# Performance work log

Hardware: AMD Instinct MI355X
Metric: run time of the kernel (lower is better)

The kernel has to match this reference:

```python
import jax, jax.numpy as jnp
import numpy as np

EPS = 1e-10
TOP_K = 2  # experts_per_token


def setup_inputs() -> dict:
    key = jax.random.key(0)
    k1, k2 = jax.random.split(key)
    dim, E = 2048, 64
    B, S = 4, 4096
    x = jax.random.normal(k1, (B * S, dim), dtype=jnp.float32)
    W = jax.random.normal(k2, (dim, E), dtype=jnp.float32) * (1.0 / np.sqrt(dim))
    b = jnp.zeros((E,), dtype=jnp.float32)
    return {"x": x, "W": W, "b": b, "batch_size": B, "seq_len": S}


def reference(x, W, b, batch_size, seq_len):
    E = W.shape[1]
    N = x.shape[0]  # batch_size * seq_len
    # gate + softmax + clamp
    scores = jax.nn.softmax(x @ W + b, axis=1)
    scores = jnp.clip(scores, EPS, 1.0 - EPS)
    # log-odds transform and rz loss over (seq, experts) per batch
    logits = jnp.log(scores / (1.0 - scores)).reshape(batch_size, seq_len, E)
    rz_loss = jnp.mean(jax.scipy.special.logsumexp(logits, axis=(1, 2)))
    # top-k experts per token
    top_scores, sel_idx = jax.lax.top_k(scores, TOP_K)  # (N, K) each
    flat_idx = sel_idx.reshape(-1)  # (N*K,)
    # histogram of assignments per expert (torch.histc with unit bins)
    num_tokens_per_expert = jax.ops.segment_sum(
        jnp.ones_like(flat_idx, dtype=jnp.float32), flat_idx, num_segments=E)
    # stable argsort groups slots by expert id, preserving token order
    perm = jnp.argsort(flat_idx, stable=True)  # (N*K,)
    top_scores_sorted = top_scores.reshape(-1)[perm]
    token_indices_experts_sorted = perm // TOP_K
    return (top_scores_sorted, token_indices_experts_sorted,
            num_tokens_per_expert, rz_loss)
```

## Files before the change

kernel.cpp:

```cpp
#include <hip/hip_runtime.h>
#include <math.h>

#define EPS_ 1e-10f
#define MARGIN 4e-3f

typedef __attribute__((ext_vector_type(8))) short sh8;
typedef __attribute__((ext_vector_type(4))) float fx4;

__device__ __forceinline__ bool betterf(float v, int i, float w, int j) {
    return (v > w) || (v == w && i < j);
}
__device__ __forceinline__ bool betterd(double v, int i, double w, int j) {
    return (v > w) || (v == w && i < j);
}
__device__ __forceinline__ unsigned short f2bf(float f) {
    unsigned u = __float_as_uint(f);
    u += 0x7fffu + ((u >> 16) & 1u);
    return (unsigned short)(u >> 16);
}
__device__ __forceinline__ float bf2f(unsigned short h) {
    return __uint_as_float(((unsigned)h) << 16);
}
__device__ __forceinline__ void cvt8(const float4 a, const float4 c, sh8& hi, sh8& lo) {
    const float v[8] = {a.x, a.y, a.z, a.w, c.x, c.y, c.z, c.w};
#pragma unroll
    for (int j = 0; j < 8; ++j) {
        const unsigned short h = f2bf(v[j]);
        hi[j] = (short)h;
        lo[j] = (short)f2bf(v[j] - bf2f(h));
    }
}
__device__ __forceinline__ void gload_lds16(const void* g, void* l) {
    __builtin_amdgcn_global_load_lds(
        (const __attribute__((address_space(1))) void*)g,
        (__attribute__((address_space(3))) void*)l, 16, 0, 0);
}

__global__ __launch_bounds__(256)
void wconv(const float* __restrict__ W, unsigned short* __restrict__ wf)
{
    const int gid = blockIdx.x * 256 + threadIdx.x;
    const int e = gid & 63, k = gid >> 6;
    const int s = k >> 5, kk = k & 31, bq = kk >> 3, j = kk & 7;
    const int t = e >> 4, n = e & 15;
    const int l = n + 16 * bq;
    const float w = W[(size_t)k * 64 + e];
    const unsigned short hi = f2bf(w);
    const unsigned short lo = f2bf(w - bf2f(hi));
    const size_t base = ((size_t)s * 4 + t) * 2;
    wf[(base + 0) * 512 + l * 8 + j] = hi;
    wf[(base + 1) * 512 + l * 8 + j] = lo;
}

#define KSPL 4
__global__ __launch_bounds__(256, 4)
void gemm_mfma(const float* __restrict__ x, const unsigned short* __restrict__ wfg,
               int dim, int N, float* __restrict__ zpart)
{
    __shared__ __align__(16) char xs[2][8192];
    __shared__ __align__(16) char wls[2][8192];

    const int tid  = threadIdx.x;
    const int lane = tid & 63;
    const int wv   = tid >> 6;
    const int rgs  = N / 64;
    const int ks   = blockIdx.x / rgs;
    const int rg   = blockIdx.x % rgs;
    const int r0   = rg * 64;
    const int kslice = dim / KSPL;
    const int k0   = ks * kslice;
    const int nstep = kslice / 32;

    const int m = lane & 15;
    const int q = lane >> 4;
    const int arow = wv * 16 + m;
    const int mk = m & 7;

    const int srow_in = lane >> 3;
    const int sgc     = (lane & 7) ^ (srow_in & 7);

    fx4 acc[4] = {};

    const char* wbytes = (const char*)wfg;
    const size_t wstep0 = (size_t)(k0 >> 5) * 8192;

#pragma unroll
    for (int r = 0; r < 2; ++r) {
        const int row = wv * 16 + r * 8 + srow_in;
        gload_lds16(x + (size_t)(r0 + row) * dim + k0 + sgc * 4,
                    &xs[0][(wv * 16 + r * 8) * 128]);
        gload_lds16(wbytes + wstep0 + wv * 2048 + r * 1024 + lane * 16,
                    &wls[0][wv * 2048 + r * 1024]);
    }
    __syncthreads();

    for (int s = 0; s < nstep; ++s) {
        const int cb = s & 1;
        if (s + 1 < nstep) {
#pragma unroll
            for (int r = 0; r < 2; ++r) {
                const int row = wv * 16 + r * 8 + srow_in;
                gload_lds16(x + (size_t)(r0 + row) * dim + k0 + (s + 1) * 32 + sgc * 4,
                            &xs[cb ^ 1][(wv * 16 + r * 8) * 128]);
                gload_lds16(wbytes + wstep0 + (size_t)(s + 1) * 8192
                                  + wv * 2048 + r * 1024 + lane * 16,
                            &wls[cb ^ 1][wv * 2048 + r * 1024]);
            }
        }
        {
            const float4 f0 = *(const float4*)&xs[cb][arow * 128 + ((2 * q + 0) ^ mk) * 16];
            const float4 f1 = *(const float4*)&xs[cb][arow * 128 + ((2 * q + 1) ^ mk) * 16];
            sh8 ah, al;
            cvt8(f0, f1, ah, al);
#pragma unroll
            for (int te = 0; te < 4; ++te) {
                const sh8 bh = __builtin_bit_cast(sh8,
                    *(const int4*)&wls[cb][(te * 2 + 0) * 1024 + lane * 16]);
                const sh8 bl = __builtin_bit_cast(sh8,
                    *(const int4*)&wls[cb][(te * 2 + 1) * 1024 + lane * 16]);
                acc[te] = __builtin_amdgcn_mfma_f32_16x16x32_bf16(ah, bh, acc[te], 0, 0, 0);
                acc[te] = __builtin_amdgcn_mfma_f32_16x16x32_bf16(ah, bl, acc[te], 0, 0, 0);
                acc[te] = __builtin_amdgcn_mfma_f32_16x16x32_bf16(al, bh, acc[te], 0, 0, 0);
            }
        }
        __syncthreads();
    }

    const int n = lane & 15;
    const int g = lane >> 4;
    float* zp = zpart + ((size_t)ks * N + r0 + wv * 16) * 64;
#pragma unroll
    for (int te = 0; te < 4; ++te)
#pragma unroll
        for (int i = 0; i < 4; ++i)
            zp[(g * 4 + i) * 64 + te * 16 + n] = acc[te][i];
}

__global__ __launch_bounds__(256)
void merge_epi32(const float* __restrict__ zpart, const float* __restrict__ b,
                 const int* __restrict__ sl_p, int N, int nchunks,
                 float* __restrict__ ts, int* __restrict__ sel,
                 int* __restrict__ nflags, int* __restrict__ flaglist,
                 int* __restrict__ hist, int* __restrict__ cnt2,
                 double* __restrict__ bsum)
{
    __shared__ int cnt[64];
    __shared__ float rsum[4];

    const int tid  = threadIdx.x;
    const int lane = tid & 63;
    const int wv   = tid >> 6;
    const int c    = blockIdx.x;
    const int e    = lane;
    const float be = b[e];

    if (tid < 64) cnt[tid] = 0;
    __syncthreads();

    float myrz = 0.0f;

    for (int rr = 0; rr < 8; ++rr) {
        const int row = c * 32 + wv * 8 + rr;
        float z = be;
#pragma unroll
        for (int ks = 0; ks < KSPL; ++ks)
            z += zpart[((size_t)ks * N + row) * 64 + e];

        float v1 = z, v2 = -3.4e38f;
        int i1 = e, i2 = 1 << 30;
#pragma unroll
        for (int mm = 1; mm < 64; mm <<= 1) {
            const float wva = __shfl_xor(v1, mm, 64); const int j1 = __shfl_xor(i1, mm, 64);
            const float wvb = __shfl_xor(v2, mm, 64); const int j2 = __shfl_xor(i2, mm, 64);
            if (betterf(wva, j1, v1, i1)) {
                float nv2; int ni2;
                if (betterf(v1, i1, wvb, j2)) { nv2 = v1; ni2 = i1; }
                else                          { nv2 = wvb; ni2 = j2; }
                v1 = wva; i1 = j1; v2 = nv2; i2 = ni2;
            } else if (betterf(wva, j1, v2, i2)) { v2 = wva; i2 = j1; }
        }

        float m3 = (e == i1 || e == i2) ? -3.4e38f : z;
#pragma unroll
        for (int mm = 1; mm < 64; mm <<= 1) m3 = fmaxf(m3, __shfl_xor(m3, mm, 64));

        const float ex = expf(z - v1);
        float ssum = ex;
#pragma unroll
        for (int mm = 1; mm < 64; mm <<= 1) ssum += __shfl_xor(ssum, mm, 64);
        const float inv = 1.0f / ssum;

        float sc = fminf(fmaxf(ex * inv, EPS_), 1.0f - EPS_);
        float srz = sc / (1.0f - sc);
#pragma unroll
        for (int mm = 1; mm < 64; mm <<= 1) srz += __shfl_xor(srz, mm, 64);

        if (e == 0) {
            const float s1 = fminf(fmaxf(inv, EPS_), 1.0f - EPS_);
            const float s2 = fminf(fmaxf(expf(v2 - v1) * inv, EPS_), 1.0f - EPS_);
            ts[row * 2 + 0] = s1;
            ts[row * 2 + 1] = s2;
            sel[row * 2 + 0] = i1;
            sel[row * 2 + 1] = i2;
            atomicAdd(&cnt[i1], 1);
            atomicAdd(&cnt[i2], 1);
            myrz += srz;
            if ((v1 - v2) < MARGIN || (v2 - m3) < MARGIN) {
                const int slot = atomicAdd(nflags, 1);
                flaglist[slot] = row;
            }
        }
    }

    if (lane == 0) rsum[wv] = myrz;
    __syncthreads();

    if (tid < 64) {
        cnt2[(size_t)tid * nchunks + c] = cnt[tid];
        if (cnt[tid]) atomicAdd(&hist[tid], cnt[tid]);
    }
    if (tid == 0) {
        const int seq = sl_p[0];
        const int batch = (c * 32) / seq;
        atomicAdd(&bsum[batch], (double)(rsum[0] + rsum[1] + rsum[2] + rsum[3]));
    }
}

__global__ __launch_bounds__(1024)
void fixup(const float* __restrict__ x, const float* __restrict__ W,
           const float* __restrict__ b, int dim, int nchunks,
           const int* __restrict__ nflags, const int* __restrict__ flaglist,
           float* __restrict__ ts, int* __restrict__ sel,
           int* __restrict__ hist, int* __restrict__ cnt2)
{
    __shared__ double red[1024];
    const int tid = threadIdx.x;
    const int e = tid & 63;
    const int q = tid >> 6;
    const int nf = *nflags;
    const int slice = dim >> 4;

    for (int f = blockIdx.x; f < nf; f += gridDim.x) {
        const int row = flaglist[f];
        const float* xr = x + (size_t)row * dim;
        const int k0 = q * slice;
        double a0 = 0.0, a1 = 0.0, a2 = 0.0, a3 = 0.0;
        for (int k = k0; k < k0 + slice; k += 4) {
            a0 = fma((double)xr[k + 0], (double)W[(size_t)(k + 0) * 64 + e], a0);
            a1 = fma((double)xr[k + 1], (double)W[(size_t)(k + 1) * 64 + e], a1);
            a2 = fma((double)xr[k + 2], (double)W[(size_t)(k + 2) * 64 + e], a2);
            a3 = fma((double)xr[k + 3], (double)W[(size_t)(k + 3) * 64 + e], a3);
        }
        red[tid] = (a0 + a1) + (a2 + a3);
        __syncthreads();
        for (int st = 512; st >= 64; st >>= 1) {
            if (tid < st) red[tid] += red[tid + st];
            __syncthreads();
        }
        if (tid < 64) {
            const double z = red[tid] + (double)b[e];
            double v1 = z, v2 = -1e300;
            int i1 = e, i2 = 1 << 30;
#pragma unroll
            for (int mm = 1; mm < 64; mm <<= 1) {
                const double w1 = __shfl_xor(v1, mm, 64); const int j1 = __shfl_xor(i1, mm, 64);
                const double w2 = __shfl_xor(v2, mm, 64); const int j2 = __shfl_xor(i2, mm, 64);
                if (betterd(w1, j1, v1, i1)) {
                    double nv2; int ni2;
                    if (betterd(v1, i1, w2, j2)) { nv2 = v1; ni2 = i1; }
                    else                         { nv2 = w2; ni2 = j2; }
                    v1 = w1; i1 = j1; v2 = nv2; i2 = ni2;
                } else if (betterd(w1, j1, v2, i2)) { v2 = w1; i2 = j1; }
            }
            float sl = expf((float)(z - v1));
            float ssum = sl;
#pragma unroll
            for (int mm = 1; mm < 64; mm <<= 1) ssum += __shfl_xor(ssum, mm, 64);
            const float inv = 1.0f / ssum;
            if (e == 0) {
                const float s1 = fminf(fmaxf(inv, EPS_), 1.0f - EPS_);
                const float s2 = fminf(fmaxf(expf((float)(v2 - v1)) * inv, EPS_), 1.0f - EPS_);
                const int o1 = sel[row * 2 + 0];
                const int o2 = sel[row * 2 + 1];
                ts[row * 2 + 0] = s1;
                ts[row * 2 + 1] = s2;
                if (o1 != i1 || o2 != i2) {
                    sel[row * 2 + 0] = i1;
                    sel[row * 2 + 1] = i2;
                    const int c = row >> 5;
                    atomicSub(&hist[o1], 1); atomicSub(&hist[o2], 1);
                    atomicAdd(&hist[i1], 1); atomicAdd(&hist[i2], 1);
                    atomicSub(&cnt2[(size_t)o1 * nchunks + c], 1);
                    atomicSub(&cnt2[(size_t)o2 * nchunks + c], 1);
                    atomicAdd(&cnt2[(size_t)i1 * nchunks + c], 1);
                    atomicAdd(&cnt2[(size_t)i2 * nchunks + c], 1);
                }
            }
        }
        __syncthreads();
    }
}

__global__ __launch_bounds__(1024)
void scan2(const int* __restrict__ hist, const int* __restrict__ cnt2,
           int nchunks, int* __restrict__ cbase,
           const double* __restrict__ bsum, const int* __restrict__ bs_p,
           float* __restrict__ out_cnt, float* __restrict__ out_rz)
{
    __shared__ int sc[1024];
    __shared__ int es;
    const int e = blockIdx.x;
    const int t = threadIdx.x;

    if (t == 0) {
        int s = 0;
        for (int i = 0; i < e; ++i) s += hist[i];
        es = s;
        out_cnt[e] = (float)hist[e];
        if (e == 0) {
            const int nb = bs_p[0];
            double a = 0.0;
            for (int i = 0; i < nb; ++i) a += log(bsum[i]);
            out_rz[0] = (float)(a / nb);
        }
    }
    const int v = (t < nchunks) ? cnt2[(size_t)e * nchunks + t] : 0;
    sc[t] = v;
    __syncthreads();
#pragma unroll
    for (int off = 1; off < 1024; off <<= 1) {
        const int add = (t >= off) ? sc[t - off] : 0;
        __syncthreads();
        sc[t] += add;
        __syncthreads();
    }
    if (t < nchunks)
        cbase[(size_t)t * 64 + e] = es + sc[t] - v;
}

__global__ void scatter(const int* __restrict__ sel, const float* __restrict__ ts,
                        const int* __restrict__ cbase,
                        float* __restrict__ out_sc, float* __restrict__ out_idx)
{
    __shared__ int shx[64];
    const int lane = threadIdx.x;
    const int c = blockIdx.x;
    const int idx = c * 64 + lane;
    const int ex = sel[idx];
    shx[lane] = ex;
    __syncthreads();
    int pre = 0;
#pragma unroll
    for (int j = 0; j < 64; ++j) pre += (int)((j < lane) && (shx[j] == ex));
    const int pos = cbase[c * 64 + ex] + pre;
    out_sc[pos]  = ts[idx];
    out_idx[pos] = (float)(idx >> 1);
}

extern "C" void kernel_launch(void* const* d_in, const int* in_sizes, int n_in,
                              void* d_out, int out_size, void* d_ws, size_t ws_size,
                              hipStream_t stream)
{
    const float* x = (const float*)d_in[0];
    const float* W = (const float*)d_in[1];
    const float* b = (const float*)d_in[2];
    const int* bs_p = (const int*)d_in[3];
    const int* sl_p = (const int*)d_in[4];

    const int E   = in_sizes[2];
    const int dim = in_sizes[1] / E;
    const int N   = in_sizes[0] / dim;
    const int total = N * 2;
    const int nchunks = total / 64;

    char* ws = (char*)d_ws;
    size_t off = 0;
    int*    hist     = (int*)(ws + off); off += 256;
    double* bsum     = (double*)(ws + off); off += 512;
    int*    nflags   = (int*)(ws + off); off += 256;
    float*  ts       = (float*)(ws + off); off += (size_t)total * 4;
    int*    sel      = (int*)(ws + off); off += (size_t)total * 4;
    int*    flaglist = (int*)(ws + off); off += (size_t)N * 4;
    int*    cnt2     = (int*)(ws + off); off += (size_t)nchunks * 64 * 4;
    int*    cbase    = (int*)(ws + off); off += (size_t)nchunks * 64 * 4;
    unsigned short* wfg = (unsigned short*)(ws + off); off += (size_t)dim * 64 * 2 * 2;
    float*  zpart    = (float*)(ws + off); off += (size_t)KSPL * N * 64 * 4;

    float* out_sc  = (float*)d_out;
    float* out_idx = out_sc + total;
    float* out_cnt = out_idx + total;
    float* out_rz  = out_cnt + E;

    hipMemsetAsync(ws, 0, 1024, stream);

    hipLaunchKernelGGL(wconv, dim3(dim * 64 / 256), dim3(256), 0, stream, W, wfg);
    hipLaunchKernelGGL(gemm_mfma, dim3((N / 64) * KSPL), dim3(256), 0, stream,
                       x, wfg, dim, N, zpart);
    hipLaunchKernelGGL(merge_epi32, dim3(nchunks), dim3(256), 0, stream,
                       zpart, b, sl_p, N, nchunks, ts, sel, nflags, flaglist,
                       hist, cnt2, bsum);
    hipLaunchKernelGGL(fixup, dim3(512), dim3(1024), 0, stream,
                       x, W, b, dim, nchunks, nflags, flaglist, ts, sel, hist, cnt2);
    hipLaunchKernelGGL(scan2, dim3(64), dim3(1024), 0, stream,
                       hist, cnt2, nchunks, cbase, bsum, bs_p, out_cnt, out_rz);
    hipLaunchKernelGGL(scatter, dim3(nchunks), dim3(64), 0, stream,
                       sel, ts, cbase, out_sc, out_idx);
}
```

Measured before the change: 90.78 us.

## Triple-buffer GEMM LDS staging with explicit vmcnt waits and raw barriers

Switches the gate GEMM from double to triple buffering of x and W tiles in LDS. Loads now run two stages ahead, and each step waits on a partial vmcnt instead of draining every outstanding load with __syncthreads. The goal is to hide more global-memory latency behind the MFMA work. In exchange, LDS use per block grows from 32KB to 48KB and the occupancy hint drops from 4 to 3 blocks. The hand-counted vmcnt values also depend on exactly how many loads each stage issues.

Result: slower. 97.56 us (+7.5%).

```diff
diff --git a/kernel.cpp b/kernel.cpp
--- a/kernel.cpp
+++ b/kernel.cpp
@@ -53,12 +53,11 @@
 }
 
 #define KSPL 4
-__global__ __launch_bounds__(256, 4)
+__global__ __launch_bounds__(256, 3)
 void gemm_mfma(const float* __restrict__ x, const unsigned short* __restrict__ wfg,
                int dim, int N, float* __restrict__ zpart)
 {
-    __shared__ __align__(16) char xs[2][8192];
-    __shared__ __align__(16) char wls[2][8192];
+    __shared__ __align__(16) char smem[3][16384];
 
     const int tid  = threadIdx.x;
     const int lane = tid & 63;
@@ -84,47 +83,55 @@
     const char* wbytes = (const char*)wfg;
     const size_t wstep0 = (size_t)(k0 >> 5) * 8192;
 
-#pragma unroll
-    for (int r = 0; r < 2; ++r) {
-        const int row = wv * 16 + r * 8 + srow_in;
-        gload_lds16(x + (size_t)(r0 + row) * dim + k0 + sgc * 4,
-                    &xs[0][(wv * 16 + r * 8) * 128]);
-        gload_lds16(wbytes + wstep0 + wv * 2048 + r * 1024 + lane * 16,
-                    &wls[0][wv * 2048 + r * 1024]);
-    }
-    __syncthreads();
+#define STAGE(T, BI)                                                          \
+    {                                                                         \
+        _Pragma("unroll")                                                     \
+        for (int r = 0; r < 2; ++r) {                                         \
+            const int row = wv * 16 + r * 8 + srow_in;                        \
+            gload_lds16(x + (size_t)(r0 + row) * dim + k0 + (T) * 32 + sgc * 4,\
+                        &smem[BI][(wv * 16 + r * 8) * 128]);                  \
+            gload_lds16(wbytes + wstep0 + (size_t)(T) * 8192                  \
+                              + wv * 2048 + r * 1024 + lane * 16,             \
+                        &smem[BI][8192 + wv * 2048 + r * 1024]);              \
+        }                                                                     \
+    }
+
+    STAGE(0, 0)
+    STAGE(1, 1)
 
     for (int s = 0; s < nstep; ++s) {
-        const int cb = s & 1;
-        if (s + 1 < nstep) {
-#pragma unroll
-            for (int r = 0; r < 2; ++r) {
-                const int row = wv * 16 + r * 8 + srow_in;
-                gload_lds16(x + (size_t)(r0 + row) * dim + k0 + (s + 1) * 32 + sgc * 4,
-                            &xs[cb ^ 1][(wv * 16 + r * 8) * 128]);
-                gload_lds16(wbytes + wstep0 + (size_t)(s + 1) * 8192
-                                  + wv * 2048 + r * 1024 + lane * 16,
-                            &wls[cb ^ 1][wv * 2048 + r * 1024]);
-            }
-        }
+        if (s + 2 < nstep) {
+            const int bi2 = (s + 2) % 3;
+            STAGE(s + 2, bi2)
+        }
+        const int rem = nstep - 1 - s;
+        if (rem >= 2)      asm volatile("s_waitcnt vmcnt(8)" ::: "memory");
+        else if (rem == 1) asm volatile("s_waitcnt vmcnt(4)" ::: "memory");
+        else               asm volatile("s_waitcnt vmcnt(0)" ::: "memory");
+        __builtin_amdgcn_s_barrier();
+        asm volatile("" ::: "memory");
+
         {
-            const float4 f0 = *(const float4*)&xs[cb][arow * 128 + ((2 * q + 0) ^ mk) * 16];
-            const float4 f1 = *(const float4*)&xs[cb][arow * 128 + ((2 * q + 1) ^ mk) * 16];
+            const char* buf = smem[s % 3];
+            const float4 f0 = *(const float4*)&buf[arow * 128 + ((2 * q + 0) ^ mk) * 16];
+            const float4 f1 = *(const float4*)&buf[arow * 128 + ((2 * q + 1) ^ mk) * 16];
             sh8 ah, al;
             cvt8(f0, f1, ah, al);
 #pragma unroll
             for (int te = 0; te < 4; ++te) {
                 const sh8 bh = __builtin_bit_cast(sh8,
-                    *(const int4*)&wls[cb][(te * 2 + 0) * 1024 + lane * 16]);
+                    *(const int4*)&buf[8192 + (te * 2 + 0) * 1024 + lane * 16]);
                 const sh8 bl = __builtin_bit_cast(sh8,
-                    *(const int4*)&wls[cb][(te * 2 + 1) * 1024 + lane * 16]);
+                    *(const int4*)&buf[8192 + (te * 2 + 1) * 1024 + lane * 16]);
                 acc[te] = __builtin_amdgcn_mfma_f32_16x16x32_bf16(ah, bh, acc[te], 0, 0, 0);
                 acc[te] = __builtin_amdgcn_mfma_f32_16x16x32_bf16(ah, bl, acc[te], 0, 0, 0);
                 acc[te] = __builtin_amdgcn_mfma_f32_16x16x32_bf16(al, bh, acc[te], 0, 0, 0);
             }
         }
-        __syncthreads();
-    }
+        asm volatile("" ::: "memory");
+        __builtin_amdgcn_s_barrier();
+    }
+#undef STAGE
 
     const int n = lane & 15;
     const int g = lane >> 4;
```

## Fuse split-K merge epilogue into GEMM via last-block-arrives counter

Applied to the files above, without the earlier changes.

Removes the separate merge_epi32 launch. Each GEMM block atomically increments a per-row-group counter after writing its partial sums, and the last of the KSPL blocks for that row group reduces the partials and runs the softmax/top-2/histogram/rz epilogue. This saves a kernel launch and lets the epilogue start as soon as each row group finishes. In exchange, it adds threadfence and atomic overhead, and the epilogue runs on only a quarter of the blocks, each handling 64 rows.

After: 227.6 us. 151% more time.

```diff
diff --git a/kernel.cpp b/kernel.cpp
--- a/kernel.cpp
+++ b/kernel.cpp
@@ -55,10 +55,18 @@
 #define KSPL 4
 __global__ __launch_bounds__(256, 4)
 void gemm_mfma(const float* __restrict__ x, const unsigned short* __restrict__ wfg,
-               int dim, int N, float* __restrict__ zpart)
+               const float* __restrict__ b, const int* __restrict__ sl_p,
+               int dim, int N, int nchunks, float* __restrict__ zpart,
+               float* __restrict__ ts, int* __restrict__ sel,
+               int* __restrict__ nflags, int* __restrict__ flaglist,
+               int* __restrict__ hist, int* __restrict__ cnt2,
+               double* __restrict__ bsum, int* __restrict__ done)
 {
     __shared__ __align__(16) char xs[2][8192];
     __shared__ __align__(16) char wls[2][8192];
+    __shared__ int cnt[2][64];
+    __shared__ float rsum[4];
+    __shared__ int lastflag;
 
     const int tid  = threadIdx.x;
     const int lane = tid & 63;
@@ -134,37 +142,28 @@
 #pragma unroll
         for (int i = 0; i < 4; ++i)
             zp[(g * 4 + i) * 64 + te * 16 + n] = acc[te][i];
-}
-
-__global__ __launch_bounds__(256)
-void merge_epi32(const float* __restrict__ zpart, const float* __restrict__ b,
-                 const int* __restrict__ sl_p, int N, int nchunks,
-                 float* __restrict__ ts, int* __restrict__ sel,
-                 int* __restrict__ nflags, int* __restrict__ flaglist,
-                 int* __restrict__ hist, int* __restrict__ cnt2,
-                 double* __restrict__ bsum)
-{
-    __shared__ int cnt[64];
-    __shared__ float rsum[4];
-
-    const int tid  = threadIdx.x;
-    const int lane = tid & 63;
-    const int wv   = tid >> 6;
-    const int c    = blockIdx.x;
-    const int e    = lane;
+
+    if (tid < 128) cnt[tid >> 6][tid & 63] = 0;
+    __threadfence();
+    if (tid == 0) {
+        const int old = atomicAdd(&done[rg], 1);
+        lastflag = (old == KSPL - 1);
+    }
+    __syncthreads();
+    if (!lastflag) return;
+    __threadfence();
+
+    const int e = lane;
     const float be = b[e];
-
-    if (tid < 64) cnt[tid] = 0;
-    __syncthreads();
-
+    const int lc = wv >> 1;
     float myrz = 0.0f;
 
-    for (int rr = 0; rr < 8; ++rr) {
-        const int row = c * 32 + wv * 8 + rr;
+    for (int rr = 0; rr < 16; ++rr) {
+        const int row = r0 + wv * 16 + rr;
         float z = be;
 #pragma unroll
-        for (int ks = 0; ks < KSPL; ++ks)
-            z += zpart[((size_t)ks * N + row) * 64 + e];
+        for (int s2 = 0; s2 < KSPL; ++s2)
+            z += zpart[((size_t)s2 * N + row) * 64 + e];
 
         float v1 = z, v2 = -3.4e38f;
         int i1 = e, i2 = 1 << 30;
@@ -197,13 +196,13 @@
 
         if (e == 0) {
             const float s1 = fminf(fmaxf(inv, EPS_), 1.0f - EPS_);
-            const float s2 = fminf(fmaxf(expf(v2 - v1) * inv, EPS_), 1.0f - EPS_);
+            const float s2v = fminf(fmaxf(expf(v2 - v1) * inv, EPS_), 1.0f - EPS_);
             ts[row * 2 + 0] = s1;
-            ts[row * 2 + 1] = s2;
+            ts[row * 2 + 1] = s2v;
             sel[row * 2 + 0] = i1;
             sel[row * 2 + 1] = i2;
-            atomicAdd(&cnt[i1], 1);
-            atomicAdd(&cnt[i2], 1);
+            atomicAdd(&cnt[lc][i1], 1);
+            atomicAdd(&cnt[lc][i2], 1);
             myrz += srz;
             if ((v1 - v2) < MARGIN || (v2 - m3) < MARGIN) {
                 const int slot = atomicAdd(nflags, 1);
@@ -215,13 +214,16 @@
     if (lane == 0) rsum[wv] = myrz;
     __syncthreads();
 
-    if (tid < 64) {
-        cnt2[(size_t)tid * nchunks + c] = cnt[tid];
-        if (cnt[tid]) atomicAdd(&hist[tid], cnt[tid]);
+    if (tid < 128) {
+        const int ee = tid & 63;
+        const int cc = tid >> 6;
+        const int gc2 = rg * 2 + cc;
+        cnt2[(size_t)ee * nchunks + gc2] = cnt[cc][ee];
+        if (cnt[cc][ee]) atomicAdd(&hist[ee], cnt[cc][ee]);
     }
     if (tid == 0) {
         const int seq = sl_p[0];
-        const int batch = (c * 32) / seq;
+        const int batch = r0 / seq;
         atomicAdd(&bsum[batch], (double)(rsum[0] + rsum[1] + rsum[2] + rsum[3]));
     }
 }
@@ -378,6 +380,7 @@
     int*    hist     = (int*)(ws + off); off += 256;
     double* bsum     = (double*)(ws + off); off += 512;
     int*    nflags   = (int*)(ws + off); off += 256;
+    int*    done     = (int*)(ws + off); off += (size_t)(N / 64) * 4;
     float*  ts       = (float*)(ws + off); off += (size_t)total * 4;
     int*    sel      = (int*)(ws + off); off += (size_t)total * 4;
     int*    flaglist = (int*)(ws + off); off += (size_t)N * 4;
@@ -391,14 +394,12 @@
     float* out_cnt = out_idx + total;
     float* out_rz  = out_cnt + E;
 
-    hipMemsetAsync(ws, 0, 1024, stream);
+    hipMemsetAsync(ws, 0, 1024 + (size_t)(N / 64) * 4, stream);
 
     hipLaunchKernelGGL(wconv, dim3(dim * 64 / 256), dim3(256), 0, stream, W, wfg);
     hipLaunchKernelGGL(gemm_mfma, dim3((N / 64) * KSPL), dim3(256), 0, stream,
-                       x, wfg, dim, N, zpart);
-    hipLaunchKernelGGL(merge_epi32, dim3(nchunks), dim3(256), 0, stream,
-                       zpart, b, sl_p, N, nchunks, ts, sel, nflags, flaglist,
-                       hist, cnt2, bsum);
+                       x, wfg, b, sl_p, dim, N, nchunks, zpart,
+                       ts, sel, nflags, flaglist, hist, cnt2, bsum, done);
     hipLaunchKernelGGL(fixup, dim3(512), dim3(1024), 0, stream,
                        x, W, b, dim, nchunks, nflags, flaglist, ts, sel, hist, cnt2);
     hipLaunchKernelGGL(scan2, dim3(64), dim3(1024), 0, stream,
```
